# Kernel optimization log

Measured on AMD Instinct MI355X. Metric: run time of the kernel, lower is better.

The kernel has to match this reference:

```python
import jax, jax.numpy as jnp
import numpy as np

NUM_HEADS = 12
EPS = 1e-12  # F.normalize default eps


def setup_inputs() -> dict:
    key = jax.random.key(0)
    ks = jax.random.split(key, 6)
    B, N, C, M = 32, 1024, 768, 64
    s = 1.0 / np.sqrt(C)
    return {
        "x": jax.random.normal(ks[0], (B, N, C), jnp.float32),
        "Wc": jax.random.normal(ks[1], (M, C), jnp.float32) * s,
        "bc": jnp.zeros((M,), jnp.float32),
        "Wq": jax.random.normal(ks[2], (C, C), jnp.float32) * s,
        "bq": jnp.zeros((C,), jnp.float32),
        "Wk": jax.random.normal(ks[3], (C, C), jnp.float32) * s,
        "bk": jnp.zeros((C,), jnp.float32),
        "Wv": jax.random.normal(ks[4], (C, C), jnp.float32) * s,
        "bv": jnp.zeros((C,), jnp.float32),
        "Wp": jax.random.normal(ks[5], (C, C), jnp.float32) * s,
        "bp": jnp.zeros((C,), jnp.float32),
    }


def reference(x, Wc, bc, Wq, bq, Wk, bk, Wv, bv, Wp, bp):
    B, N, C = x.shape
    H = NUM_HEADS
    D = C // H
    scale = D ** -0.5

    # Cluster: linear -> transpose -> sigmoid/N -> einsum -> L2 norm
    c = jnp.einsum('bnc,mc->bmn', x, Wc) + bc[None, :, None]   # (B, M, N)
    c = jax.nn.sigmoid(c) / N
    z = jnp.einsum('bmn,bnc->bmc', c, x)                        # (B, M, C)
    z = z / jnp.maximum(jnp.linalg.norm(z, axis=-1, keepdims=True), EPS)

    M = z.shape[1]
    q = (x @ Wq.T + bq).reshape(B, N, H, D).transpose(0, 2, 1, 3)  # (B,H,N,D)
    k = (z @ Wk.T + bk).reshape(B, M, H, D).transpose(0, 2, 1, 3)  # (B,H,M,D)
    v = (z @ Wv.T + bv).reshape(B, M, H, D).transpose(0, 2, 1, 3)  # (B,H,M,D)

    attn = jax.nn.softmax(jnp.einsum('bhnd,bhmd->bhnm', q, k) * scale, axis=-1)
    o = jnp.einsum('bhnm,bhmd->bhnd', attn, v)                  # (B,H,N,D)
    o = o.transpose(0, 2, 1, 3).reshape(B, N, C)
    return o @ Wp.T + bp
```

## Files before the change

kernel.cpp:

```cpp
#include <hip/hip_runtime.h>
#include <hip/hip_bf16.h>
#include <cstdint>

#define BB 32
#define NN 1024
#define CC 768
#define MM 64
#define HH 12
#define DD 64

typedef float f4v __attribute__((ext_vector_type(4)));
typedef __bf16 bf8 __attribute__((ext_vector_type(8)));
typedef __bf16 bf4 __attribute__((ext_vector_type(4)));

__device__ __forceinline__ f4v mfma16(bf8 a, bf8 b, f4v c) {
    return __builtin_amdgcn_mfma_f32_16x16x32_bf16(a, b, c, 0, 0, 0);
}
__device__ __forceinline__ __bf16 f2bf(float f) { return (__bf16)f; }

__device__ __forceinline__ void gl2lds16(const void* g, void* lds) {
    __builtin_amdgcn_global_load_lds((const __attribute__((address_space(1))) void*)g,
                                     (__attribute__((address_space(3))) void*)lds, 16, 0, 0);
}

__global__ __launch_bounds__(256) void k_cvtW(
        const float* __restrict__ Wc, const float* __restrict__ Wq,
        const float* __restrict__ Wk, const float* __restrict__ Wv,
        const float* __restrict__ Wp,
        __bf16* __restrict__ wc, __bf16* __restrict__ wq,
        __bf16* __restrict__ wk, __bf16* __restrict__ wv,
        __bf16* __restrict__ wp) {
    const float* in; __bf16* out; int n4;
    switch (blockIdx.y) {
        case 0: in = Wc; out = wc; n4 = MM * CC / 4; break;
        case 1: in = Wq; out = wq; n4 = CC * CC / 4; break;
        case 2: in = Wk; out = wk; n4 = CC * CC / 4; break;
        case 3: in = Wv; out = wv; n4 = CC * CC / 4; break;
        default: in = Wp; out = wp; n4 = CC * CC / 4; break;
    }
    int i = blockIdx.x * 256 + threadIdx.x;
    if (i < n4) {
        float4 v = *(const float4*)&in[i * 4];
        bf4 o; o[0] = f2bf(v.x); o[1] = f2bf(v.y); o[2] = f2bf(v.z); o[3] = f2bf(v.w);
        *(bf4*)&out[i * 4] = o;
    }
}

#define TS 80
__global__ __launch_bounds__(256) void k_cvtx(const float* __restrict__ x,
        __bf16* __restrict__ xb, __bf16* __restrict__ xt) {
    int c0 = blockIdx.x * 64, n0 = blockIdx.y * 64, b = blockIdx.z;
    __shared__ __align__(16) __bf16 tile[64 * TS];
    int t = threadIdx.x;
#pragma unroll
    for (int i = 0; i < 4; i++) {
        int idx = t + 256 * i, r = idx >> 4, cq = idx & 15;
        float4 v = *(const float4*)&x[((size_t)(b * NN + n0 + r)) * CC + c0 + cq * 4];
        __bf16* d = &tile[r * TS + cq * 4];
        d[0] = f2bf(v.x); d[1] = f2bf(v.y); d[2] = f2bf(v.z); d[3] = f2bf(v.w);
    }
    __syncthreads();
#pragma unroll
    for (int i = 0; i < 2; i++) {
        int idx = t + 256 * i, r = idx >> 3, ch = idx & 7;
        *(bf8*)&xb[((size_t)(b * NN + n0 + r)) * CC + c0 + ch * 8] = *(const bf8*)&tile[r * TS + ch * 8];
    }
#pragma unroll
    for (int i = 0; i < 2; i++) {
        int idx = t + 256 * i, c = idx >> 3, ch = idx & 7;
        bf8 v;
#pragma unroll
        for (int j = 0; j < 8; j++) v[j] = tile[(ch * 8 + j) * TS + c];
        *(bf8*)&xt[((size_t)(b * CC + c0 + c)) * NN + n0 + ch * 8] = v;
    }
}

__global__ __launch_bounds__(256) void k_cluster(const __bf16* __restrict__ xb,
        const __bf16* __restrict__ Wc, const float* __restrict__ bc,
        __bf16* __restrict__ cbmn) {
    int n0 = blockIdx.x * 128, b = blockIdx.y;
    int t = threadIdx.x, w = t >> 6, l = t & 63, quad = l >> 4, l16 = l & 15;
    f4v acc[2][4];
#pragma unroll
    for (int i = 0; i < 2; i++) for (int j = 0; j < 4; j++) acc[i][j] = (f4v)0.0f;
    for (int k0 = 0; k0 < CC; k0 += 32) {
        bf8 afr[2], bfr[4];
#pragma unroll
        for (int sr = 0; sr < 2; sr++)
            afr[sr] = *(const bf8*)&xb[((size_t)(b * NN + n0 + w * 32 + sr * 16 + l16)) * CC + k0 + quad * 8];
#pragma unroll
        for (int sc = 0; sc < 4; sc++)
            bfr[sc] = *(const bf8*)&Wc[(size_t)(sc * 16 + l16) * CC + k0 + quad * 8];
#pragma unroll
        for (int sr = 0; sr < 2; sr++)
#pragma unroll
            for (int sc = 0; sc < 4; sc++)
                acc[sr][sc] = mfma16(afr[sr], bfr[sc], acc[sr][sc]);
    }
#pragma unroll
    for (int sr = 0; sr < 2; sr++)
#pragma unroll
        for (int sc = 0; sc < 4; sc++) {
            int m = sc * 16 + l16;
            float bias = bc[m];
            bf4 p;
#pragma unroll
            for (int r = 0; r < 4; r++) {
                float val = acc[sr][sc][r] + bias;
                val = 1.0f / (1.0f + __expf(-val));
                p[r] = f2bf(val * (1.0f / 1024.0f));
            }
            *(bf4*)&cbmn[((size_t)(b * MM + m)) * NN + n0 + w * 32 + sr * 16 + quad * 4] = p;
        }
}

__global__ __launch_bounds__(256) void k_z(const __bf16* __restrict__ cbmn,
        const __bf16* __restrict__ xt, float* __restrict__ z) {
    int c0 = blockIdx.x * 64, b = blockIdx.y;
    int t = threadIdx.x, w = t >> 6, l = t & 63, quad = l >> 4, l16 = l & 15;
    f4v acc[4];
#pragma unroll
    for (int j = 0; j < 4; j++) acc[j] = (f4v)0.0f;
    for (int n0 = 0; n0 < NN; n0 += 32) {
        bf8 afr = *(const bf8*)&cbmn[((size_t)(b * MM + w * 16 + l16)) * NN + n0 + quad * 8];
#pragma unroll
        for (int sc = 0; sc < 4; sc++) {
            bf8 bfr = *(const bf8*)&xt[((size_t)(b * CC + c0 + sc * 16 + l16)) * NN + n0 + quad * 8];
            acc[sc] = mfma16(afr, bfr, acc[sc]);
        }
    }
#pragma unroll
    for (int sc = 0; sc < 4; sc++) {
        int cc = c0 + sc * 16 + l16;
#pragma unroll
        for (int r = 0; r < 4; r++) {
            int m = w * 16 + quad * 4 + r;
            z[((size_t)(b * MM + m)) * CC + cc] = acc[sc][r];
        }
    }
}

__global__ __launch_bounds__(256) void k_znorm(const float* __restrict__ z, __bf16* __restrict__ zb) {
    int w = threadIdx.x >> 6, l = threadIdx.x & 63;
    int row = blockIdx.x * 4 + w;
    const float* zr = &z[(size_t)row * CC];
    float v[12]; float ss = 0.f;
#pragma unroll
    for (int i = 0; i < 12; i++) { v[i] = zr[l + i * 64]; ss += v[i] * v[i]; }
#pragma unroll
    for (int off = 32; off; off >>= 1) ss += __shfl_xor(ss, off);
    float s = 1.0f / fmaxf(sqrtf(ss), 1e-12f);
    __bf16* zo = &zb[(size_t)row * CC];
#pragma unroll
    for (int i = 0; i < 12; i++) zo[l + i * 64] = f2bf(v[i] * s);
}

__global__ __launch_bounds__(256) void k_kv(const __bf16* __restrict__ zb,
        const __bf16* __restrict__ Wk, const float* __restrict__ bk,
        const __bf16* __restrict__ Wv, const float* __restrict__ bv,
        __bf16* __restrict__ kout, __bf16* __restrict__ vtout) {
    int ct = blockIdx.x, b = blockIdx.y, which = blockIdx.z;
    const __bf16* W = which ? Wv : Wk;
    const float* bias = which ? bv : bk;
    int t = threadIdx.x, w = t >> 6, l = t & 63, quad = l >> 4, l16 = l & 15;
    f4v acc[4][2];
#pragma unroll
    for (int i = 0; i < 4; i++) for (int j = 0; j < 2; j++) acc[i][j] = (f4v)0.0f;
    for (int k0 = 0; k0 < CC; k0 += 32) {
        bf8 afr[4], bfr[2];
#pragma unroll
        for (int sr = 0; sr < 4; sr++)
            afr[sr] = *(const bf8*)&zb[((size_t)(b * MM + sr * 16 + l16)) * CC + k0 + quad * 8];
#pragma unroll
        for (int sc = 0; sc < 2; sc++)
            bfr[sc] = *(const bf8*)&W[((size_t)(ct * 128 + w * 32 + sc * 16 + l16)) * CC + k0 + quad * 8];
#pragma unroll
        for (int sr = 0; sr < 4; sr++)
#pragma unroll
            for (int sc = 0; sc < 2; sc++)
                acc[sr][sc] = mfma16(afr[sr], bfr[sc], acc[sr][sc]);
    }
#pragma unroll
    for (int sr = 0; sr < 4; sr++)
#pragma unroll
        for (int sc = 0; sc < 2; sc++) {
            int col = ct * 128 + w * 32 + sc * 16 + l16;
            float bb = bias[col];
            int h = col >> 6, d = col & 63;
            if (which == 0) {
#pragma unroll
                for (int r = 0; r < 4; r++) {
                    int m = sr * 16 + quad * 4 + r;
                    kout[(((size_t)(b * HH + h)) * MM + m) * DD + d] = f2bf(acc[sr][sc][r] + bb);
                }
            } else {
                bf4 p;
#pragma unroll
                for (int r = 0; r < 4; r++) p[r] = f2bf(acc[sr][sc][r] + bb);
                *(bf4*)&vtout[(((size_t)(b * HH + h)) * DD + d) * MM + sr * 16 + quad * 4] = p;
            }
        }
}

#define STAGE_AB(Asrc, Bsrc, dstbase, kk)                                                             \
    do {                                                                                              \
        __bf16* _Ad = (dstbase);                                                                      \
        int _row = w * 16 + (l >> 2), _ch = (l & 3) ^ ((l >> 3) & 3);                                 \
        gl2lds16(&(Asrc)[(arow0 + _row) * CC + (kk) + _ch * 8], &_Ad[w * 512]);                       \
        gl2lds16(&(Asrc)[(arow0 + 64 + _row) * CC + (kk) + _ch * 8], &_Ad[2048 + w * 512]);           \
        gl2lds16(&(Bsrc)[((size_t)(jt * 128) + _row) * CC + (kk) + _ch * 8], &_Ad[4096 + w * 512]);   \
        gl2lds16(&(Bsrc)[((size_t)(jt * 128) + 64 + _row) * CC + (kk) + _ch * 8], &_Ad[4096 + 2048 + w * 512]); \
    } while (0)

#define GEMM_KLOOP(Asrc, Bsrc)                                                                        \
    STAGE_AB(Asrc, Bsrc, smem, 0);                                                                    \
    STAGE_AB(Asrc, Bsrc, smem + 8192, 32);                                                            \
    _Pragma("unroll")                                                                                 \
    for (int kt = 0; kt < 24; ++kt) {                                                                 \
        if (kt < 22) STAGE_AB(Asrc, Bsrc, smem + ((kt + 2) % 3) * 8192, (kt + 2) * 32);               \
        if (kt < 22)      asm volatile("s_waitcnt vmcnt(8)" ::: "memory");                            \
        else if (kt == 22) asm volatile("s_waitcnt vmcnt(4)" ::: "memory");                           \
        else               asm volatile("s_waitcnt vmcnt(0)" ::: "memory");                           \
        __builtin_amdgcn_s_barrier();                                                                 \
        const __bf16* As = smem + (kt % 3) * 8192;                                                    \
        const __bf16* Bs = As + 4096;                                                                 \
        bf8 afr[4], bfr[4];                                                                           \
        _Pragma("unroll")                                                                             \
        for (int sr = 0; sr < 4; sr++)                                                                \
            afr[sr] = *(const bf8*)&As[(wr * 64 + sr * 16 + l16) * 32 + swz * 8];                     \
        _Pragma("unroll")                                                                             \
        for (int sc = 0; sc < 4; sc++)                                                                \
            bfr[sc] = *(const bf8*)&Bs[(wc * 64 + sc * 16 + l16) * 32 + swz * 8];                     \
        __builtin_amdgcn_s_setprio(1);                                                                \
        _Pragma("unroll")                                                                             \
        for (int sr = 0; sr < 4; sr++)                                                                \
            _Pragma("unroll")                                                                         \
            for (int sc = 0; sc < 4; sc++)                                                            \
                acc[sr][sc] = mfma16(afr[sr], bfr[sc], acc[sr][sc]);                                  \
        __builtin_amdgcn_s_setprio(0);                                                                \
        __builtin_amdgcn_s_barrier();                                                                 \
    }

__global__ __launch_bounds__(256, 3) void k_qproj(const __bf16* __restrict__ xb,
        const __bf16* __restrict__ Wq, const float* __restrict__ bq,
        __bf16* __restrict__ qb) {
    int orig = blockIdx.y * gridDim.x + blockIdx.x;
    int lid = (orig & 7) * 192 + (orig >> 3);
    int jt = lid % 6;
    size_t arow0 = (size_t)(lid / 6) * 128;

    __shared__ __align__(16) __bf16 smem[3 * 8192];
    int t = threadIdx.x, w = t >> 6, l = t & 63, quad = l >> 4, l16 = l & 15;
    int wr = w & 1, wc = w >> 1;
    int swz = quad ^ ((l16 >> 1) & 3);
    f4v acc[4][4];
#pragma unroll
    for (int i = 0; i < 4; i++) for (int j = 0; j < 4; j++) acc[i][j] = (f4v)0.0f;

    GEMM_KLOOP(xb, Wq);

    __bf16* eb = smem;
    for (int p = 0; p < 2; ++p) {
        if (wc == p) {
#pragma unroll
            for (int sc = 0; sc < 4; sc++) {
                int col = jt * 128 + p * 64 + sc * 16 + l16;
                float bb = bq[col];
#pragma unroll
                for (int sr = 0; sr < 4; sr++)
#pragma unroll
                    for (int r = 0; r < 4; r++)
                        eb[(wr * 64 + sr * 16 + quad * 4 + r) * 72 + sc * 16 + l16] = f2bf(acc[sr][sc][r] + bb);
            }
        }
        __syncthreads();
#pragma unroll
        for (int i = 0; i < 4; i++) {
            int idx = t + 256 * i, row = idx >> 3, ch = idx & 7;
            *(bf8*)&qb[(arow0 + row) * CC + jt * 128 + p * 64 + ch * 8] = *(const bf8*)&eb[row * 72 + ch * 8];
        }
        __syncthreads();
    }
}

#define QS 72
__global__ __launch_bounds__(256) void k_attn(const __bf16* __restrict__ qb,
        const __bf16* __restrict__ kb, const __bf16* __restrict__ vt,
        __bf16* __restrict__ ob) {
    int n0 = blockIdx.x * 128, h = blockIdx.y, b = blockIdx.z;
    __shared__ __align__(16) __bf16 ps[128 * QS];
    int t = threadIdx.x, w = t >> 6, l = t & 63, quad = l >> 4, l16 = l & 15;
    size_t bh = (size_t)(b * HH + h);

    f4v sacc[2][4];
#pragma unroll
    for (int i = 0; i < 2; i++) for (int j = 0; j < 4; j++) sacc[i][j] = (f4v)0.0f;
#pragma unroll
    for (int kc = 0; kc < 2; kc++) {
        bf8 afr[2], bfr[4];
#pragma unroll
        for (int sr = 0; sr < 2; sr++)
            afr[sr] = *(const bf8*)&qb[((size_t)(b * NN + n0 + w * 32 + sr * 16 + l16)) * CC + h * 64 + kc * 32 + quad * 8];
#pragma unroll
        for (int sc = 0; sc < 4; sc++)
            bfr[sc] = *(const bf8*)&kb[(bh * MM + sc * 16 + l16) * DD + kc * 32 + quad * 8];
#pragma unroll
        for (int sr = 0; sr < 2; sr++)
#pragma unroll
            for (int sc = 0; sc < 4; sc++)
                sacc[sr][sc] = mfma16(afr[sr], bfr[sc], sacc[sr][sc]);
    }
#pragma unroll
    for (int sr = 0; sr < 2; sr++) {
#pragma unroll
        for (int r = 0; r < 4; r++) {
            float mx = -1e30f;
#pragma unroll
            for (int sc = 0; sc < 4; sc++) mx = fmaxf(mx, sacc[sr][sc][r] * 0.125f);
#pragma unroll
            for (int off = 1; off < 16; off <<= 1) mx = fmaxf(mx, __shfl_xor(mx, off));
            float e[4]; float sum = 0.f;
#pragma unroll
            for (int sc = 0; sc < 4; sc++) { e[sc] = __expf(sacc[sr][sc][r] * 0.125f - mx); sum += e[sc]; }
#pragma unroll
            for (int off = 1; off < 16; off <<= 1) sum += __shfl_xor(sum, off);
            float inv = 1.0f / sum;
            int row = w * 32 + sr * 16 + quad * 4 + r;
#pragma unroll
            for (int sc = 0; sc < 4; sc++) ps[row * QS + sc * 16 + l16] = f2bf(e[sc] * inv);
        }
    }
    f4v oacc[2][4];
#pragma unroll
    for (int i = 0; i < 2; i++) for (int j = 0; j < 4; j++) oacc[i][j] = (f4v)0.0f;
#pragma unroll
    for (int kc = 0; kc < 2; kc++) {
        bf8 afr[2], bfr[4];
#pragma unroll
        for (int sr = 0; sr < 2; sr++)
            afr[sr] = *(const bf8*)&ps[(w * 32 + sr * 16 + l16) * QS + kc * 32 + quad * 8];
#pragma unroll
        for (int sc = 0; sc < 4; sc++)
            bfr[sc] = *(const bf8*)&vt[(bh * DD + sc * 16 + l16) * MM + kc * 32 + quad * 8];
#pragma unroll
        for (int sr = 0; sr < 2; sr++)
#pragma unroll
            for (int sc = 0; sc < 4; sc++)
                oacc[sr][sc] = mfma16(afr[sr], bfr[sc], oacc[sr][sc]);
    }
#pragma unroll
    for (int sr = 0; sr < 2; sr++)
#pragma unroll
        for (int sc = 0; sc < 4; sc++) {
            int row = w * 32 + sr * 16;
#pragma unroll
            for (int r = 0; r < 4; r++)
                ps[(row + quad * 4 + r) * QS + sc * 16 + l16] = f2bf(oacc[sr][sc][r]);
        }
    __syncthreads();
#pragma unroll
    for (int i = 0; i < 4; i++) {
        int idx = t + 256 * i, row = idx >> 3, ch = idx & 7;
        *(bf8*)&ob[((size_t)(b * NN + n0 + row)) * CC + h * 64 + ch * 8] = *(const bf8*)&ps[row * QS + ch * 8];
    }
}

__global__ __launch_bounds__(256, 3) void k_oproj(const __bf16* __restrict__ ob,
        const __bf16* __restrict__ Wp, const float* __restrict__ bp,
        float* __restrict__ out) {
    int orig = blockIdx.y * gridDim.x + blockIdx.x;
    int lid = (orig & 7) * 192 + (orig >> 3);
    int jt = lid % 6;
    size_t arow0 = (size_t)(lid / 6) * 128;

    __shared__ __align__(16) __bf16 smem[3 * 8192];
    int t = threadIdx.x, w = t >> 6, l = t & 63, quad = l >> 4, l16 = l & 15;
    int wr = w & 1, wc = w >> 1;
    int swz = quad ^ ((l16 >> 1) & 3);
    f4v acc[4][4];
#pragma unroll
    for (int i = 0; i < 4; i++) for (int j = 0; j < 4; j++) acc[i][j] = (f4v)0.0f;

    GEMM_KLOOP(ob, Wp);

    float* eb = (float*)smem;
    for (int p = 0; p < 2; ++p) {
        if (wc == p) {
#pragma unroll
            for (int sc = 0; sc < 4; sc++) {
                int col = jt * 128 + p * 64 + sc * 16 + l16;
                float bb = bp[col];
#pragma unroll
                for (int sr = 0; sr < 4; sr++)
#pragma unroll
                    for (int r = 0; r < 4; r++)
                        eb[(wr * 64 + sr * 16 + quad * 4 + r) * 68 + sc * 16 + l16] = acc[sr][sc][r] + bb;
            }
        }
        __syncthreads();
#pragma unroll
        for (int i = 0; i < 8; i++) {
            int idx = t + 256 * i, row = idx >> 4, c4 = idx & 15;
            *(float4*)&out[(arow0 + row) * CC + jt * 128 + p * 64 + c4 * 4] = *(const float4*)&eb[row * 68 + c4 * 4];
        }
        __syncthreads();
    }
}

extern "C" void kernel_launch(void* const* d_in, const int* in_sizes, int n_in,
                              void* d_out, int out_size, void* d_ws, size_t ws_size,
                              hipStream_t stream) {
    (void)in_sizes; (void)n_in; (void)out_size; (void)ws_size;
    const float* x  = (const float*)d_in[0];
    const float* Wc = (const float*)d_in[1];
    const float* bc = (const float*)d_in[2];
    const float* Wq = (const float*)d_in[3];
    const float* bq = (const float*)d_in[4];
    const float* Wk = (const float*)d_in[5];
    const float* bk = (const float*)d_in[6];
    const float* Wv = (const float*)d_in[7];
    const float* bv = (const float*)d_in[8];
    const float* Wp = (const float*)d_in[9];
    const float* bp = (const float*)d_in[10];
    float* out = (float*)d_out;

    char* ws = (char*)d_ws;
    size_t off = 0;
    auto alloc = [&](size_t bytes) { void* p = ws + off; off = (off + bytes + 255) & ~(size_t)255; return p; };
    __bf16* wc_b = (__bf16*)alloc((size_t)MM * CC * 2);
    __bf16* wq_b = (__bf16*)alloc((size_t)CC * CC * 2);
    __bf16* wk_b = (__bf16*)alloc((size_t)CC * CC * 2);
    __bf16* wv_b = (__bf16*)alloc((size_t)CC * CC * 2);
    __bf16* wp_b = (__bf16*)alloc((size_t)CC * CC * 2);
    __bf16* xb   = (__bf16*)alloc((size_t)BB * NN * CC * 2);
    __bf16* xt_o = (__bf16*)alloc((size_t)BB * NN * CC * 2);
    __bf16* q_b  = (__bf16*)alloc((size_t)BB * NN * CC * 2);
    __bf16* c_bmn= (__bf16*)alloc((size_t)BB * MM * NN * 2);
    float*  z_f  = (float*) alloc((size_t)BB * MM * CC * 4);
    __bf16* z_b  = (__bf16*)alloc((size_t)BB * MM * CC * 2);
    __bf16* k_b  = (__bf16*)alloc((size_t)BB * HH * MM * DD * 2);
    __bf16* v_t  = (__bf16*)alloc((size_t)BB * HH * MM * DD * 2);

    k_cvtW<<<dim3((CC * CC / 4 + 255) / 256, 5), 256, 0, stream>>>(
        Wc, Wq, Wk, Wv, Wp, wc_b, wq_b, wk_b, wv_b, wp_b);

    k_cvtx<<<dim3(CC / 64, NN / 64, BB), 256, 0, stream>>>(x, xb, xt_o);
    k_cluster<<<dim3(NN / 128, BB), 256, 0, stream>>>(xb, wc_b, bc, c_bmn);
    k_z<<<dim3(CC / 64, BB), 256, 0, stream>>>(c_bmn, xt_o, z_f);
    k_znorm<<<(BB * MM) / 4, 256, 0, stream>>>(z_f, z_b);
    k_kv<<<dim3(CC / 128, BB, 2), 256, 0, stream>>>(z_b, wk_b, bk, wv_b, bv, k_b, v_t);
    k_qproj<<<dim3(CC / 128, (BB * NN) / 128), 256, 0, stream>>>(xb, wq_b, bq, q_b);
    k_attn<<<dim3(NN / 128, HH, BB), 256, 0, stream>>>(q_b, k_b, v_t, xt_o );
    k_oproj<<<dim3(CC / 128, (BB * NN) / 128), 256, 0, stream>>>(xt_o, wp_b, bp, out);
}
```

Measured before the change: 271.4 us.

## Retile projection GEMMs to 256x128 with BK=64 and swizzle x transpose

```diff
diff --git a/kernel.cpp b/kernel.cpp
--- a/kernel.cpp
+++ b/kernel.cpp
@@ -50,28 +50,32 @@
 __global__ __launch_bounds__(256) void k_cvtx(const float* __restrict__ x,
         __bf16* __restrict__ xb, __bf16* __restrict__ xt) {
     int c0 = blockIdx.x * 64, n0 = blockIdx.y * 64, b = blockIdx.z;
-    __shared__ __align__(16) __bf16 tile[64 * TS];
+    __shared__ __align__(16) __bf16 tileR[64 * TS];
+    __shared__ __align__(16) __bf16 tileC[64 * 64];
     int t = threadIdx.x;
 #pragma unroll
     for (int i = 0; i < 4; i++) {
         int idx = t + 256 * i, r = idx >> 4, cq = idx & 15;
         float4 v = *(const float4*)&x[((size_t)(b * NN + n0 + r)) * CC + c0 + cq * 4];
-        __bf16* d = &tile[r * TS + cq * 4];
-        d[0] = f2bf(v.x); d[1] = f2bf(v.y); d[2] = f2bf(v.z); d[3] = f2bf(v.w);
+        float vv[4] = {v.x, v.y, v.z, v.w};
+        __bf16* d = &tileR[r * TS + cq * 4];
+#pragma unroll
+        for (int j = 0; j < 4; j++) {
+            __bf16 bv = f2bf(vv[j]);
+            d[j] = bv;
+            int cl = cq * 4 + j;
+            int s = (cl ^ (cl >> 2)) & 7;
+            tileC[cl * 64 + (((r >> 3) ^ s) << 3) + (r & 7)] = bv;
+        }
     }
     __syncthreads();
 #pragma unroll
     for (int i = 0; i < 2; i++) {
         int idx = t + 256 * i, r = idx >> 3, ch = idx & 7;
-        *(bf8*)&xb[((size_t)(b * NN + n0 + r)) * CC + c0 + ch * 8] = *(const bf8*)&tile[r * TS + ch * 8];
-    }
-#pragma unroll
-    for (int i = 0; i < 2; i++) {
-        int idx = t + 256 * i, c = idx >> 3, ch = idx & 7;
-        bf8 v;
-#pragma unroll
-        for (int j = 0; j < 8; j++) v[j] = tile[(ch * 8 + j) * TS + c];
-        *(bf8*)&xt[((size_t)(b * CC + c0 + c)) * NN + n0 + ch * 8] = v;
+        *(bf8*)&xb[((size_t)(b * NN + n0 + r)) * CC + c0 + ch * 8] = *(const bf8*)&tileR[r * TS + ch * 8];
+        int s = (r ^ (r >> 2)) & 7;
+        bf8 v2 = *(const bf8*)&tileC[r * 64 + ((ch ^ s) << 3)];
+        *(bf8*)&xt[((size_t)(b * CC + c0 + r)) * NN + n0 + ch * 8] = v2;
     }
 }
 
@@ -202,66 +206,79 @@
         }
 }
 
-#define STAGE_AB(Asrc, Bsrc, dstbase, kk)                                                             \
+#define STAGE8(Asrc, Bsrc, buf, kk)                                                                   \
     do {                                                                                              \
-        __bf16* _Ad = (dstbase);                                                                      \
-        int _row = w * 16 + (l >> 2), _ch = (l & 3) ^ ((l >> 3) & 3);                                 \
-        gl2lds16(&(Asrc)[(arow0 + _row) * CC + (kk) + _ch * 8], &_Ad[w * 512]);                       \
-        gl2lds16(&(Asrc)[(arow0 + 64 + _row) * CC + (kk) + _ch * 8], &_Ad[2048 + w * 512]);           \
-        gl2lds16(&(Bsrc)[((size_t)(jt * 128) + _row) * CC + (kk) + _ch * 8], &_Ad[4096 + w * 512]);   \
-        gl2lds16(&(Bsrc)[((size_t)(jt * 128) + 64 + _row) * CC + (kk) + _ch * 8], &_Ad[4096 + 2048 + w * 512]); \
+        __bf16* _d = (buf);                                                                           \
+        int _r8 = l >> 3, _gkc = (l & 7) ^ _r8;                                                       \
+        _Pragma("unroll")                                                                             \
+        for (int _a = 0; _a < 4; _a++) {                                                              \
+            int _ra = w * 4 + _a; int _row = _ra * 8 + _r8;                                           \
+            gl2lds16(&(Asrc)[(arow0 + _row) * CC + (kk) + _gkc * 8], &_d[_ra * 512]);                 \
+        }                                                                                             \
+        _Pragma("unroll")                                                                             \
+        for (int _bq = 0; _bq < 2; _bq++) {                                                           \
+            int _rb = w * 2 + _bq; int _row = _rb * 8 + _r8;                                          \
+            gl2lds16(&(Bsrc)[((size_t)(jt * 128) + _row) * CC + (kk) + _gkc * 8],                     \
+                     &_d[16384 + _rb * 512]);                                                         \
+        }                                                                                             \
     } while (0)
 
-#define GEMM_KLOOP(Asrc, Bsrc)                                                                        \
-    STAGE_AB(Asrc, Bsrc, smem, 0);                                                                    \
-    STAGE_AB(Asrc, Bsrc, smem + 8192, 32);                                                            \
-    _Pragma("unroll")                                                                                 \
-    for (int kt = 0; kt < 24; ++kt) {                                                                 \
-        if (kt < 22) STAGE_AB(Asrc, Bsrc, smem + ((kt + 2) % 3) * 8192, (kt + 2) * 32);               \
-        if (kt < 22)      asm volatile("s_waitcnt vmcnt(8)" ::: "memory");                            \
-        else if (kt == 22) asm volatile("s_waitcnt vmcnt(4)" ::: "memory");                           \
+#define GEMM_KLOOP8(Asrc, Bsrc)                                                                       \
+    STAGE8(Asrc, Bsrc, smem, 0);                                                                      \
+    STAGE8(Asrc, Bsrc, smem + 24576, 64);                                                             \
+    for (int kt = 0; kt < 12; ++kt) {                                                                 \
+        if (kt < 10) STAGE8(Asrc, Bsrc, smem + ((kt + 2) % 3) * 24576, (kt + 2) * 64);                \
+        if (kt < 10)       asm volatile("s_waitcnt vmcnt(12)" ::: "memory");                          \
+        else if (kt == 10) asm volatile("s_waitcnt vmcnt(6)" ::: "memory");                           \
         else               asm volatile("s_waitcnt vmcnt(0)" ::: "memory");                           \
         __builtin_amdgcn_s_barrier();                                                                 \
-        const __bf16* As = smem + (kt % 3) * 8192;                                                    \
-        const __bf16* Bs = As + 4096;                                                                 \
-        bf8 afr[4], bfr[4];                                                                           \
+        __builtin_amdgcn_sched_barrier(0);                                                            \
+        const __bf16* As = smem + (kt % 3) * 24576;                                                   \
+        const __bf16* Bs = As + 16384;                                                                \
         _Pragma("unroll")                                                                             \
-        for (int sr = 0; sr < 4; sr++)                                                                \
-            afr[sr] = *(const bf8*)&As[(wr * 64 + sr * 16 + l16) * 32 + swz * 8];                     \
-        _Pragma("unroll")                                                                             \
-        for (int sc = 0; sc < 4; sc++)                                                                \
-            bfr[sc] = *(const bf8*)&Bs[(wc * 64 + sc * 16 + l16) * 32 + swz * 8];                     \
-        __builtin_amdgcn_s_setprio(1);                                                                \
-        _Pragma("unroll")                                                                             \
-        for (int sr = 0; sr < 4; sr++)                                                                \
+        for (int ks = 0; ks < 2; ks++) {                                                              \
+            bf8 afr[4], bfr[4];                                                                       \
             _Pragma("unroll")                                                                         \
-            for (int sc = 0; sc < 4; sc++)                                                            \
-                acc[sr][sc] = mfma16(afr[sr], bfr[sc], acc[sr][sc]);                                  \
-        __builtin_amdgcn_s_setprio(0);                                                                \
+            for (int sr = 0; sr < 4; sr++) {                                                          \
+                int row = wm * 64 + sr * 16 + l16;                                                    \
+                afr[sr] = *(const bf8*)&As[row * 64 + (((ks << 2) | quad) ^ (row & 7)) * 8];          \
+            }                                                                                         \
+            _Pragma("unroll")                                                                         \
+            for (int sc = 0; sc < 4; sc++) {                                                          \
+                int row = wn * 64 + sc * 16 + l16;                                                    \
+                bfr[sc] = *(const bf8*)&Bs[row * 64 + (((ks << 2) | quad) ^ (row & 7)) * 8];          \
+            }                                                                                         \
+            __builtin_amdgcn_s_setprio(1);                                                            \
+            _Pragma("unroll")                                                                         \
+            for (int sr = 0; sr < 4; sr++)                                                            \
+                _Pragma("unroll")                                                                     \
+                for (int sc = 0; sc < 4; sc++)                                                        \
+                    acc[sr][sc] = mfma16(afr[sr], bfr[sc], acc[sr][sc]);                              \
+            __builtin_amdgcn_s_setprio(0);                                                            \
+        }                                                                                             \
         __builtin_amdgcn_s_barrier();                                                                 \
     }
 
-__global__ __launch_bounds__(256, 3) void k_qproj(const __bf16* __restrict__ xb,
+__global__ __launch_bounds__(512, 2) void k_qproj(const __bf16* __restrict__ xb,
         const __bf16* __restrict__ Wq, const float* __restrict__ bq,
         __bf16* __restrict__ qb) {
-    int orig = blockIdx.y * gridDim.x + blockIdx.x;
-    int lid = (orig & 7) * 192 + (orig >> 3);
+    int orig = blockIdx.x;
+    int lid = (orig & 7) * 96 + (orig >> 3);
     int jt = lid % 6;
-    size_t arow0 = (size_t)(lid / 6) * 128;
-
-    __shared__ __align__(16) __bf16 smem[3 * 8192];
-    int t = threadIdx.x, w = t >> 6, l = t & 63, quad = l >> 4, l16 = l & 15;
-    int wr = w & 1, wc = w >> 1;
-    int swz = quad ^ ((l16 >> 1) & 3);
+    size_t arow0 = (size_t)(lid / 6) * 256;
+
+    __shared__ __align__(16) __bf16 smem[3 * 24576];
+    int t = threadIdx.x, w = t >> 6, l = t & 63, quad = l >> 4, l16 = l & 15;
+    int wm = w >> 1, wn = w & 1;
     f4v acc[4][4];
 #pragma unroll
     for (int i = 0; i < 4; i++) for (int j = 0; j < 4; j++) acc[i][j] = (f4v)0.0f;
 
-    GEMM_KLOOP(xb, Wq);
+    GEMM_KLOOP8(xb, Wq);
 
     __bf16* eb = smem;
     for (int p = 0; p < 2; ++p) {
-        if (wc == p) {
+        if (wn == p) {
 #pragma unroll
             for (int sc = 0; sc < 4; sc++) {
                 int col = jt * 128 + p * 64 + sc * 16 + l16;
@@ -270,13 +287,13 @@
                 for (int sr = 0; sr < 4; sr++)
 #pragma unroll
                     for (int r = 0; r < 4; r++)
-                        eb[(wr * 64 + sr * 16 + quad * 4 + r) * 72 + sc * 16 + l16] = f2bf(acc[sr][sc][r] + bb);
+                        eb[(wm * 64 + sr * 16 + quad * 4 + r) * 72 + sc * 16 + l16] = f2bf(acc[sr][sc][r] + bb);
             }
         }
         __syncthreads();
 #pragma unroll
         for (int i = 0; i < 4; i++) {
-            int idx = t + 256 * i, row = idx >> 3, ch = idx & 7;
+            int idx = t + 512 * i, row = idx >> 3, ch = idx & 7;
             *(bf8*)&qb[(arow0 + row) * CC + jt * 128 + p * 64 + ch * 8] = *(const bf8*)&eb[row * 72 + ch * 8];
         }
         __syncthreads();
@@ -365,27 +382,26 @@
     }
 }
 
-__global__ __launch_bounds__(256, 3) void k_oproj(const __bf16* __restrict__ ob,
+__global__ __launch_bounds__(512, 2) void k_oproj(const __bf16* __restrict__ ob,
         const __bf16* __restrict__ Wp, const float* __restrict__ bp,
         float* __restrict__ out) {
-    int orig = blockIdx.y * gridDim.x + blockIdx.x;
-    int lid = (orig & 7) * 192 + (orig >> 3);
+    int orig = blockIdx.x;
+    int lid = (orig & 7) * 96 + (orig >> 3);
     int jt = lid % 6;
-    size_t arow0 = (size_t)(lid / 6) * 128;
-
-    __shared__ __align__(16) __bf16 smem[3 * 8192];
-    int t = threadIdx.x, w = t >> 6, l = t & 63, quad = l >> 4, l16 = l & 15;
-    int wr = w & 1, wc = w >> 1;
-    int swz = quad ^ ((l16 >> 1) & 3);
+    size_t arow0 = (size_t)(lid / 6) * 256;
+
+    __shared__ __align__(16) __bf16 smem[3 * 24576];
+    int t = threadIdx.x, w = t >> 6, l = t & 63, quad = l >> 4, l16 = l & 15;
+    int wm = w >> 1, wn = w & 1;
     f4v acc[4][4];
 #pragma unroll
     for (int i = 0; i < 4; i++) for (int j = 0; j < 4; j++) acc[i][j] = (f4v)0.0f;
 
-    GEMM_KLOOP(ob, Wp);
+    GEMM_KLOOP8(ob, Wp);
 
     float* eb = (float*)smem;
     for (int p = 0; p < 2; ++p) {
-        if (wc == p) {
+        if (wn == p) {
 #pragma unroll
             for (int sc = 0; sc < 4; sc++) {
                 int col = jt * 128 + p * 64 + sc * 16 + l16;
@@ -394,13 +410,13 @@
                 for (int sr = 0; sr < 4; sr++)
 #pragma unroll
                     for (int r = 0; r < 4; r++)
-                        eb[(wr * 64 + sr * 16 + quad * 4 + r) * 68 + sc * 16 + l16] = acc[sr][sc][r] + bb;
+                        eb[(wm * 64 + sr * 16 + quad * 4 + r) * 68 + sc * 16 + l16] = acc[sr][sc][r] + bb;
             }
         }
         __syncthreads();
 #pragma unroll
         for (int i = 0; i < 8; i++) {
-            int idx = t + 256 * i, row = idx >> 4, c4 = idx & 15;
+            int idx = t + 512 * i, row = idx >> 4, c4 = idx & 15;
             *(float4*)&out[(arow0 + row) * CC + jt * 128 + p * 64 + c4 * 4] = *(const float4*)&eb[row * 68 + c4 * 4];
         }
         __syncthreads();
@@ -449,7 +465,7 @@
     k_z<<<dim3(CC / 64, BB), 256, 0, stream>>>(c_bmn, xt_o, z_f);
     k_znorm<<<(BB * MM) / 4, 256, 0, stream>>>(z_f, z_b);
     k_kv<<<dim3(CC / 128, BB, 2), 256, 0, stream>>>(z_b, wk_b, bk, wv_b, bv, k_b, v_t);
-    k_qproj<<<dim3(CC / 128, (BB * NN) / 128), 256, 0, stream>>>(xb, wq_b, bq, q_b);
+    k_qproj<<<dim3((BB * NN / 256) * (CC / 128)), 512, 0, stream>>>(xb, wq_b, bq, q_b);
     k_attn<<<dim3(NN / 128, HH, BB), 256, 0, stream>>>(q_b, k_b, v_t, xt_o );
-    k_oproj<<<dim3(CC / 128, (BB * NN) / 128), 256, 0, stream>>>(xt_o, wp_b, bp, out);
-}
+    k_oproj<<<dim3((BB * NN / 256) * (CC / 128)), 512, 0, stream>>>(xt_o, wp_b, bp, out);
+}
```

Measured after the change: 290.6 us. +7.1%, slower.

## Widen projection GEMM tiles to 128x256, load B directly from global

Applied to the files above, without the earlier changes.

```diff
diff --git a/kernel.cpp b/kernel.cpp
--- a/kernel.cpp
+++ b/kernel.cpp
@@ -46,32 +46,31 @@
     }
 }
 
-#define TS 80
 __global__ __launch_bounds__(256) void k_cvtx(const float* __restrict__ x,
         __bf16* __restrict__ xb, __bf16* __restrict__ xt) {
     int c0 = blockIdx.x * 64, n0 = blockIdx.y * 64, b = blockIdx.z;
-    __shared__ __align__(16) __bf16 tile[64 * TS];
+    __shared__ __align__(16) __bf16 tileT[64 * 66];
     int t = threadIdx.x;
 #pragma unroll
     for (int i = 0; i < 4; i++) {
         int idx = t + 256 * i, r = idx >> 4, cq = idx & 15;
         float4 v = *(const float4*)&x[((size_t)(b * NN + n0 + r)) * CC + c0 + cq * 4];
-        __bf16* d = &tile[r * TS + cq * 4];
-        d[0] = f2bf(v.x); d[1] = f2bf(v.y); d[2] = f2bf(v.z); d[3] = f2bf(v.w);
+        float vv[4] = {v.x, v.y, v.z, v.w};
+        bf4 o;
+#pragma unroll
+        for (int j = 0; j < 4; j++) {
+            __bf16 bv = f2bf(vv[j]);
+            o[j] = bv;
+            tileT[(cq * 4 + j) * 66 + r] = bv;
+        }
+        *(bf4*)&xb[((size_t)(b * NN + n0 + r)) * CC + c0 + cq * 4] = o;
     }
     __syncthreads();
-#pragma unroll
-    for (int i = 0; i < 2; i++) {
-        int idx = t + 256 * i, r = idx >> 3, ch = idx & 7;
-        *(bf8*)&xb[((size_t)(b * NN + n0 + r)) * CC + c0 + ch * 8] = *(const bf8*)&tile[r * TS + ch * 8];
-    }
 #pragma unroll
     for (int i = 0; i < 2; i++) {
         int idx = t + 256 * i, c = idx >> 3, ch = idx & 7;
-        bf8 v;
-#pragma unroll
-        for (int j = 0; j < 8; j++) v[j] = tile[(ch * 8 + j) * TS + c];
-        *(bf8*)&xt[((size_t)(b * CC + c0 + c)) * NN + n0 + ch * 8] = v;
+        bf8 v2 = *(const bf8*)&tileT[c * 66 + ch * 8];
+        *(bf8*)&xt[((size_t)(b * CC + c0 + c)) * NN + n0 + ch * 8] = v2;
     }
 }
 
@@ -202,82 +201,78 @@
         }
 }
 
-#define STAGE_AB(Asrc, Bsrc, dstbase, kk)                                                             \
-    do {                                                                                              \
-        __bf16* _Ad = (dstbase);                                                                      \
-        int _row = w * 16 + (l >> 2), _ch = (l & 3) ^ ((l >> 3) & 3);                                 \
-        gl2lds16(&(Asrc)[(arow0 + _row) * CC + (kk) + _ch * 8], &_Ad[w * 512]);                       \
-        gl2lds16(&(Asrc)[(arow0 + 64 + _row) * CC + (kk) + _ch * 8], &_Ad[2048 + w * 512]);           \
-        gl2lds16(&(Bsrc)[((size_t)(jt * 128) + _row) * CC + (kk) + _ch * 8], &_Ad[4096 + w * 512]);   \
-        gl2lds16(&(Bsrc)[((size_t)(jt * 128) + 64 + _row) * CC + (kk) + _ch * 8], &_Ad[4096 + 2048 + w * 512]); \
+#define STAGE_A(Asrc, buf, kk)                                                        \
+    do {                                                                              \
+        __bf16* _d = (buf);                                                           \
+        int _row = t >> 2, _gkc = (t & 3) ^ ((t >> 3) & 3);                           \
+        gl2lds16(&(Asrc)[(arow0 + _row) * CC + (kk) + _gkc * 8], &_d[w * 512]);       \
+        gl2lds16(&(Asrc)[(arow0 + 64 + _row) * CC + (kk) + _gkc * 8], &_d[2048 + w * 512]); \
     } while (0)
 
-#define GEMM_KLOOP(Asrc, Bsrc)                                                                        \
-    STAGE_AB(Asrc, Bsrc, smem, 0);                                                                    \
-    STAGE_AB(Asrc, Bsrc, smem + 8192, 32);                                                            \
-    _Pragma("unroll")                                                                                 \
-    for (int kt = 0; kt < 24; ++kt) {                                                                 \
-        if (kt < 22) STAGE_AB(Asrc, Bsrc, smem + ((kt + 2) % 3) * 8192, (kt + 2) * 32);               \
-        if (kt < 22)      asm volatile("s_waitcnt vmcnt(8)" ::: "memory");                            \
-        else if (kt == 22) asm volatile("s_waitcnt vmcnt(4)" ::: "memory");                           \
-        else               asm volatile("s_waitcnt vmcnt(0)" ::: "memory");                           \
-        __builtin_amdgcn_s_barrier();                                                                 \
-        const __bf16* As = smem + (kt % 3) * 8192;                                                    \
-        const __bf16* Bs = As + 4096;                                                                 \
-        bf8 afr[4], bfr[4];                                                                           \
-        _Pragma("unroll")                                                                             \
-        for (int sr = 0; sr < 4; sr++)                                                                \
-            afr[sr] = *(const bf8*)&As[(wr * 64 + sr * 16 + l16) * 32 + swz * 8];                     \
-        _Pragma("unroll")                                                                             \
-        for (int sc = 0; sc < 4; sc++)                                                                \
-            bfr[sc] = *(const bf8*)&Bs[(wc * 64 + sc * 16 + l16) * 32 + swz * 8];                     \
-        __builtin_amdgcn_s_setprio(1);                                                                \
-        _Pragma("unroll")                                                                             \
-        for (int sr = 0; sr < 4; sr++)                                                                \
-            _Pragma("unroll")                                                                         \
-            for (int sc = 0; sc < 4; sc++)                                                            \
-                acc[sr][sc] = mfma16(afr[sr], bfr[sc], acc[sr][sc]);                                  \
-        __builtin_amdgcn_s_setprio(0);                                                                \
-        __builtin_amdgcn_s_barrier();                                                                 \
-    }
-
-__global__ __launch_bounds__(256, 3) void k_qproj(const __bf16* __restrict__ xb,
+#define GEMM_KLOOP_BD(Asrc, Bsrc)                                                     \
+    STAGE_A(Asrc, smem, 0);                                                           \
+    STAGE_A(Asrc, smem + 4096, 32);                                                   \
+    asm volatile("s_waitcnt vmcnt(2)" ::: "memory");                                  \
+    __builtin_amdgcn_s_barrier();                                                     \
+    for (int kt = 0; kt < 24; ++kt) {                                                 \
+        int k0 = kt * 32;                                                             \
+        const __bf16* As = smem + (kt % 3) * 4096;                                    \
+        bf8 bfr[4], afr[8];                                                           \
+        _Pragma("unroll")                                                             \
+        for (int sc = 0; sc < 4; sc++)                                                \
+            bfr[sc] = *(const bf8*)&(Bsrc)[(size_t)(jt * 256 + w * 64 + sc * 16 + l16) * CC + k0 + quad * 8]; \
+        _Pragma("unroll")                                                             \
+        for (int sr = 0; sr < 8; sr++)                                                \
+            afr[sr] = *(const bf8*)&As[(sr * 16 + l16) * 32 + swz * 8];               \
+        __builtin_amdgcn_sched_barrier(0);                                            \
+        if (kt < 22) STAGE_A(Asrc, smem + ((kt + 2) % 3) * 4096, (kt + 2) * 32);      \
+        __builtin_amdgcn_s_setprio(1);                                                \
+        _Pragma("unroll")                                                             \
+        for (int sr = 0; sr < 8; sr++)                                                \
+            _Pragma("unroll")                                                         \
+            for (int sc = 0; sc < 4; sc++)                                            \
+                acc[sr][sc] = mfma16(afr[sr], bfr[sc], acc[sr][sc]);                  \
+        __builtin_amdgcn_s_setprio(0);                                                \
+        asm volatile("s_waitcnt vmcnt(2)" ::: "memory");                              \
+        __builtin_amdgcn_s_barrier();                                                 \
+    }
+
+__global__ __launch_bounds__(256, 2) void k_qproj(const __bf16* __restrict__ xb,
         const __bf16* __restrict__ Wq, const float* __restrict__ bq,
         __bf16* __restrict__ qb) {
-    int orig = blockIdx.y * gridDim.x + blockIdx.x;
-    int lid = (orig & 7) * 192 + (orig >> 3);
-    int jt = lid % 6;
-    size_t arow0 = (size_t)(lid / 6) * 128;
-
-    __shared__ __align__(16) __bf16 smem[3 * 8192];
-    int t = threadIdx.x, w = t >> 6, l = t & 63, quad = l >> 4, l16 = l & 15;
-    int wr = w & 1, wc = w >> 1;
+    int orig = blockIdx.x;
+    int lid = (orig & 7) * 96 + (orig >> 3);
+    int jt = lid % 3;
+    size_t arow0 = (size_t)(lid / 3) * 128;
+
+    __shared__ __align__(16) __bf16 smem[3 * 4096];
+    __shared__ __align__(16) __bf16 eb[128 * 72];
+    int t = threadIdx.x, w = t >> 6, l = t & 63, quad = l >> 4, l16 = l & 15;
     int swz = quad ^ ((l16 >> 1) & 3);
-    f4v acc[4][4];
-#pragma unroll
-    for (int i = 0; i < 4; i++) for (int j = 0; j < 4; j++) acc[i][j] = (f4v)0.0f;
-
-    GEMM_KLOOP(xb, Wq);
-
-    __bf16* eb = smem;
-    for (int p = 0; p < 2; ++p) {
-        if (wc == p) {
+    f4v acc[8][4];
+#pragma unroll
+    for (int i = 0; i < 8; i++) for (int j = 0; j < 4; j++) acc[i][j] = (f4v)0.0f;
+
+    GEMM_KLOOP_BD(xb, Wq);
+
+    for (int p = 0; p < 4; ++p) {
+        if (w == p) {
 #pragma unroll
             for (int sc = 0; sc < 4; sc++) {
-                int col = jt * 128 + p * 64 + sc * 16 + l16;
+                int col = jt * 256 + p * 64 + sc * 16 + l16;
                 float bb = bq[col];
 #pragma unroll
-                for (int sr = 0; sr < 4; sr++)
+                for (int sr = 0; sr < 8; sr++)
 #pragma unroll
                     for (int r = 0; r < 4; r++)
-                        eb[(wr * 64 + sr * 16 + quad * 4 + r) * 72 + sc * 16 + l16] = f2bf(acc[sr][sc][r] + bb);
+                        eb[(sr * 16 + quad * 4 + r) * 72 + sc * 16 + l16] = f2bf(acc[sr][sc][r] + bb);
             }
         }
         __syncthreads();
 #pragma unroll
         for (int i = 0; i < 4; i++) {
             int idx = t + 256 * i, row = idx >> 3, ch = idx & 7;
-            *(bf8*)&qb[(arow0 + row) * CC + jt * 128 + p * 64 + ch * 8] = *(const bf8*)&eb[row * 72 + ch * 8];
+            *(bf8*)&qb[(arow0 + row) * CC + jt * 256 + p * 64 + ch * 8] = *(const bf8*)&eb[row * 72 + ch * 8];
         }
         __syncthreads();
     }
@@ -365,43 +360,42 @@
     }
 }
 
-__global__ __launch_bounds__(256, 3) void k_oproj(const __bf16* __restrict__ ob,
+__global__ __launch_bounds__(256, 2) void k_oproj(const __bf16* __restrict__ ob,
         const __bf16* __restrict__ Wp, const float* __restrict__ bp,
         float* __restrict__ out) {
-    int orig = blockIdx.y * gridDim.x + blockIdx.x;
-    int lid = (orig & 7) * 192 + (orig >> 3);
-    int jt = lid % 6;
-    size_t arow0 = (size_t)(lid / 6) * 128;
-
-    __shared__ __align__(16) __bf16 smem[3 * 8192];
-    int t = threadIdx.x, w = t >> 6, l = t & 63, quad = l >> 4, l16 = l & 15;
-    int wr = w & 1, wc = w >> 1;
+    int orig = blockIdx.x;
+    int lid = (orig & 7) * 96 + (orig >> 3);
+    int jt = lid % 3;
+    size_t arow0 = (size_t)(lid / 3) * 128;
+
+    __shared__ __align__(16) __bf16 smem[3 * 4096];
+    __shared__ __align__(16) float ebf[128 * 68];
+    int t = threadIdx.x, w = t >> 6, l = t & 63, quad = l >> 4, l16 = l & 15;
     int swz = quad ^ ((l16 >> 1) & 3);
-    f4v acc[4][4];
-#pragma unroll
-    for (int i = 0; i < 4; i++) for (int j = 0; j < 4; j++) acc[i][j] = (f4v)0.0f;
-
-    GEMM_KLOOP(ob, Wp);
-
-    float* eb = (float*)smem;
-    for (int p = 0; p < 2; ++p) {
-        if (wc == p) {
+    f4v acc[8][4];
+#pragma unroll
+    for (int i = 0; i < 8; i++) for (int j = 0; j < 4; j++) acc[i][j] = (f4v)0.0f;
+
+    GEMM_KLOOP_BD(ob, Wp);
+
+    for (int p = 0; p < 4; ++p) {
+        if (w == p) {
 #pragma unroll
             for (int sc = 0; sc < 4; sc++) {
-                int col = jt * 128 + p * 64 + sc * 16 + l16;
+                int col = jt * 256 + p * 64 + sc * 16 + l16;
                 float bb = bp[col];
 #pragma unroll
-                for (int sr = 0; sr < 4; sr++)
+                for (int sr = 0; sr < 8; sr++)
 #pragma unroll
                     for (int r = 0; r < 4; r++)
-                        eb[(wr * 64 + sr * 16 + quad * 4 + r) * 68 + sc * 16 + l16] = acc[sr][sc][r] + bb;
+                        ebf[(sr * 16 + quad * 4 + r) * 68 + sc * 16 + l16] = acc[sr][sc][r] + bb;
             }
         }
         __syncthreads();
 #pragma unroll
         for (int i = 0; i < 8; i++) {
             int idx = t + 256 * i, row = idx >> 4, c4 = idx & 15;
-            *(float4*)&out[(arow0 + row) * CC + jt * 128 + p * 64 + c4 * 4] = *(const float4*)&eb[row * 68 + c4 * 4];
+            *(float4*)&out[(arow0 + row) * CC + jt * 256 + p * 64 + c4 * 4] = *(const float4*)&ebf[row * 68 + c4 * 4];
         }
         __syncthreads();
     }
@@ -449,7 +443,7 @@
     k_z<<<dim3(CC / 64, BB), 256, 0, stream>>>(c_bmn, xt_o, z_f);
     k_znorm<<<(BB * MM) / 4, 256, 0, stream>>>(z_f, z_b);
     k_kv<<<dim3(CC / 128, BB, 2), 256, 0, stream>>>(z_b, wk_b, bk, wv_b, bv, k_b, v_t);
-    k_qproj<<<dim3(CC / 128, (BB * NN) / 128), 256, 0, stream>>>(xb, wq_b, bq, q_b);
+    k_qproj<<<dim3((BB * NN / 128) * 3), 256, 0, stream>>>(xb, wq_b, bq, q_b);
     k_attn<<<dim3(NN / 128, HH, BB), 256, 0, stream>>>(q_b, k_b, v_t, xt_o );
-    k_oproj<<<dim3(CC / 128, (BB * NN) / 128), 256, 0, stream>>>(xt_o, wp_b, bp, out);
-}
+    k_oproj<<<dim3((BB * NN / 128) * 3), 256, 0, stream>>>(xt_o, wp_b, bp, out);
+}
```

Result: slower. 314.9 us (+16.0%).
